# Optimization experiments

Measured on AMD Instinct MI355X. Metric: run time of the kernel, lower is better.

Reference implementation:

```python
import jax, jax.numpy as jnp
import numpy as np

N, D, C, K = 16384, 128, 10, 16
EPS = float(np.finfo(np.float32).eps)
LOG2PI = float(np.log(2.0 * np.pi))


def setup_inputs() -> dict:
    key = jax.random.key(0)
    ks = jax.random.split(key, 8)
    X = jax.random.normal(ks[0], (N, D), dtype=jnp.float32)
    y = jax.random.randint(ks[1], (N,), 0, C, dtype=jnp.int32)
    responsibilities = jax.random.uniform(ks[2], (C, N, K), dtype=jnp.float32)
    mu = jax.random.normal(ks[3], (C, K, D), dtype=jnp.float32)
    # lower < mu < upper so the truncation normalizer is positive (as after gmm_initialisation)
    lower = mu - 1.0 + 0.1 * jax.random.normal(ks[4], (C, K, D), dtype=jnp.float32)
    upper = mu + 1.0 + 0.1 * jax.random.normal(ks[5], (C, K, D), dtype=jnp.float32)
    sigma = jnp.abs(jax.random.normal(ks[6], (C, K, D), dtype=jnp.float32))
    logits_k = jax.random.normal(ks[7], (C, K), dtype=jnp.float32)
    eta = jnp.float32(0.0)  # model initializes eta = 0.0 (non-trainable)
    return {"X": X, "y": y, "responsibilities": responsibilities, "mu": mu,
            "lower": lower, "upper": upper, "sigma": sigma,
            "logits_k": logits_k, "eta": eta}


def _stgma_loss(X, y, responsibilities, mu, lower, upper, sigma, logits_k, eta):
    # scale = eps + softplus(sigma), shape [C, K, D]
    scale = EPS + jax.nn.softplus(sigma)
    # normalizing constant per (class, component): prod_d [Phi(up) - Phi(lo)] + eps
    ndtr = jax.scipy.special.ndtr
    z = ndtr((upper - mu) / scale) - ndtr((lower - mu) / scale)       # [C, K, D]
    log_norm = jnp.log(jnp.prod(z, axis=-1) + EPS)                    # [C, K]
    log_cat = jax.nn.log_softmax(logits_k, axis=-1)                   # [C, K]

    # gather per-sample class parameters: [N, K, D]
    mu_y, lo_y, up_y, sc_y = mu[y], lower[y], upper[y], scale[y]
    xk = X[:, None, :]                                                # [N, 1, D]

    # soft truncation margins: sum_d -softplus(-eta * (x - lower)) etc.
    lp_low = -jnp.sum(jax.nn.softplus(-eta * (xk - lo_y)), axis=-1)   # [N, K]
    lp_up = -jnp.sum(jax.nn.softplus(-eta * (up_y - xk)), axis=-1)    # [N, K]

    # independent diagonal Normal log prob per component
    zd = (xk - mu_y) / sc_y
    comp_lp = jnp.sum(-0.5 * zd * zd - jnp.log(sc_y), axis=-1) - 0.5 * D * LOG2PI  # [N, K]

    log_pdf = log_cat[y] - log_norm[y] + lp_low + lp_up + comp_lp     # [N, K]

    # responsibilities for each sample from its own class
    resp = responsibilities[y, jnp.arange(N)]                         # [N, K]
    weighted = resp * log_pdf                                         # [N, K]

    # per-class reduce_mean over the class's samples and components, then -sum
    onehot = (y[:, None] == jnp.arange(C)[None, :]).astype(weighted.dtype)  # [N, C]
    class_sums = jnp.einsum('nk,nc->c', weighted, onehot)             # [C]
    counts = jnp.sum(onehot, axis=0) * K                              # [C]
    return -jnp.sum(class_sums / counts)


def reference(X, y, responsibilities, mu, lower, upper, sigma, logits_k, eta):
    return _stgma_loss(X, y, responsibilities, mu, lower, upper, sigma, logits_k, eta)
```

## Files before the change

kernel.cpp:

```cpp
#include <hip/hip_runtime.h>
#include <math.h>

#define N_PTS 16384
#define D_DIM 128
#define C_CLS 10
#define K_MIX 16
#define HIST_BLOCKS 64
#define MAIN_BPC 32

constexpr float EPSF   = 1.1920928955078125e-07f;
constexpr float LOG2PI = 1.8378770664093453f;
constexpr float LN2F   = 0.6931471805599453f;

__device__ __forceinline__ float softplusf(float x) {
    if (x > 20.f)  return x;
    if (x < -20.f) return expf(x);
    return log1pf(expf(x));
}
__device__ __forceinline__ float ndtrf(float x) {
    return 0.5f * erfcf(-x * 0.70710678118654752440f);
}

__global__ __launch_bounds__(256) void k_prep(
    const float* __restrict__ mu, const float* __restrict__ lower,
    const float* __restrict__ upper, const float* __restrict__ sigma,
    const int* __restrict__ y,
    float2* __restrict__ abT, float* __restrict__ loT, float* __restrict__ upT,
    float* __restrict__ Ack, int* __restrict__ blockCnt) {
    int b = blockIdx.x, t = threadIdx.x;
    if (b < C_CLS * K_MIX) {
        int c = b / K_MIX, k = b % K_MIX;
        __shared__ float rs0[256], rs1[256], rp[256];
        float logsc = 0.f, mu2 = 0.f, zz = 1.f;
        if (t < D_DIM) {
            int gi = b * D_DIM + t;
            float m = mu[gi], lo = lower[gi], up = upper[gi], sg = sigma[gi];
            float sc = EPSF + softplusf(sg);
            float is = 1.f / sc;
            int ti = (c * D_DIM + t) * K_MIX + k;
            abT[ti] = make_float2(is * is, 2.f * m * is * is);
            loT[ti] = lo; upT[ti] = up;
            logsc = logf(sc);
            mu2   = m * m * is * is;
            zz    = ndtrf((up - m) * is) - ndtrf((lo - m) * is);
        }
        rs0[t] = logsc; rs1[t] = mu2; rp[t] = zz;
        __syncthreads();
        for (int off = 128; off > 0; off >>= 1) {
            if (t < off) { rs0[t] += rs0[t+off]; rs1[t] += rs1[t+off]; rp[t] *= rp[t+off]; }
            __syncthreads();
        }
        if (t == 0) {
            float log_norm = logf(rp[0] + EPSF);
            Ack[b] = -log_norm - rs0[0] - 0.5f * (float)D_DIM * LOG2PI - 0.5f * rs1[0];
        }
    } else {
        int h = b - C_CLS * K_MIX;
        __shared__ int hist[C_CLS];
        if (t < C_CLS) hist[t] = 0;
        __syncthreads();
        int c = y[h * 256 + t];
        int lane = t & 63;
        for (int cc = 0; cc < C_CLS; ++cc) {
            unsigned long long m = __ballot(c == cc);
            if (lane == 0 && m) atomicAdd(&hist[cc], __popcll(m));
        }
        __syncthreads();
        if (t < C_CLS) blockCnt[h * C_CLS + t] = hist[t];
    }
}

__global__ __launch_bounds__(256) void k_scatter(
    const int* __restrict__ y, const int* __restrict__ blockCnt,
    const float* __restrict__ logits, const float* __restrict__ Ack,
    int* __restrict__ idxSorted, int* __restrict__ classOff,
    float* __restrict__ invden, float* __restrict__ const_ck) {
    __shared__ int sCnt[HIST_BLOCKS * C_CLS];
    __shared__ int sClassOff[C_CLS + 1];
    __shared__ int myOff[C_CLS];
    __shared__ int wcnt[4][C_CLS];
    __shared__ int wbase[4][C_CLS];
    int h = blockIdx.x, t = threadIdx.x;
    for (int i = t; i < HIST_BLOCKS * C_CLS; i += 256) sCnt[i] = blockCnt[i];
    __syncthreads();
    if (t == 0) {
        int acc = 0;
        for (int c = 0; c < C_CLS; ++c) {
            sClassOff[c] = acc;
            int s = 0;
            for (int hh = 0; hh < HIST_BLOCKS; ++hh) s += sCnt[hh * C_CLS + c];
            acc += s;
        }
        sClassOff[C_CLS] = acc;
    }
    __syncthreads();
    if (t < C_CLS) {
        int s = sClassOff[t];
        for (int hh = 0; hh < h; ++hh) s += sCnt[hh * C_CLS + t];
        myOff[t] = s;
    }
    __syncthreads();
    int n = h * 256 + t;
    int c = y[n];
    int w = t >> 6, lane = t & 63;
    int rank = 0;
    for (int cc = 0; cc < C_CLS; ++cc) {
        unsigned long long m = __ballot(c == cc);
        if (c == cc) rank = __popcll(m & ((1ull << lane) - 1ull));
        if (lane == 0) wcnt[w][cc] = __popcll(m);
    }
    __syncthreads();
    if (t < 4 * C_CLS) {
        int ww = t / C_CLS, cc = t % C_CLS;
        int s = myOff[cc];
        for (int w2 = 0; w2 < ww; ++w2) s += wcnt[w2][cc];
        wbase[ww][cc] = s;
    }
    __syncthreads();
    idxSorted[wbase[w][c] + rank] = n;

    if (h == 0) {
        __shared__ float lse[C_CLS];
        if (t < C_CLS) {
            float mx = -1e30f;
            for (int k = 0; k < K_MIX; ++k) mx = fmaxf(mx, logits[t * K_MIX + k]);
            float se = 0.f;
            for (int k = 0; k < K_MIX; ++k) se += expf(logits[t * K_MIX + k] - mx);
            lse[t] = mx + logf(se);
            int cnt = sClassOff[t + 1] - sClassOff[t];
            invden[t] = (cnt > 0) ? 1.f / ((float)cnt * (float)K_MIX) : 0.f;
        }
        if (t < C_CLS + 1) classOff[t] = sClassOff[t];
        __syncthreads();
        if (t < C_CLS * K_MIX) const_ck[t] = logits[t] - lse[t / K_MIX] + Ack[t];
    }
}

__global__ __launch_bounds__(256) void k_main(
    const float* __restrict__ X, const float* __restrict__ resp,
    const float2* __restrict__ abT, const float* __restrict__ loT,
    const float* __restrict__ upT, const float* __restrict__ const_ck,
    const int* __restrict__ classOff, const float* __restrict__ invden,
    const int* __restrict__ idxSorted, const float* __restrict__ etap,
    float* __restrict__ partials) {
    int b = blockIdx.x;
    int c = b / MAIN_BPC, j = b % MAIN_BPC;
    int t = threadIdx.x;
    int w = t >> 6, lane = t & 63;
    int k = lane & 15, dc = lane >> 4;
    const int d0 = dc * 32;

    float a_[32], b_[32];
    const float2* ab = abT + (size_t)c * D_DIM * K_MIX + k;
    #pragma unroll
    for (int i = 0; i < 32; ++i) {
        float2 v = ab[(size_t)(d0 + i) * K_MIX];
        a_[i] = v.x; b_[i] = v.y;
    }
    float ck  = const_ck[c * K_MIX + k];
    float eta = etap[0];
    float inv = invden[c];
    int off = classOff[c];
    int cnt = classOff[c + 1] - off;
    const float lpconst = -2.f * (float)D_DIM * LN2F;

    float wsum = 0.f;
    for (int p = j * 4 + w; p < cnt; p += MAIN_BPC * 4) {
        int n = idxSorted[off + p];
        const float* xr = X + (size_t)n * D_DIM + d0;
        float acc = 0.f, lp = lpconst;
        if (eta == 0.f) {
            #pragma unroll
            for (int i4 = 0; i4 < 8; ++i4) {
                float4 xv = *reinterpret_cast<const float4*>(xr + i4 * 4);
                acc = fmaf(xv.x, fmaf(a_[i4*4+0], xv.x, -b_[i4*4+0]), acc);
                acc = fmaf(xv.y, fmaf(a_[i4*4+1], xv.y, -b_[i4*4+1]), acc);
                acc = fmaf(xv.z, fmaf(a_[i4*4+2], xv.z, -b_[i4*4+2]), acc);
                acc = fmaf(xv.w, fmaf(a_[i4*4+3], xv.w, -b_[i4*4+3]), acc);
            }
            acc += __shfl_xor(acc, 16);
            acc += __shfl_xor(acc, 32);
        } else {
            float lpp = 0.f;
            const float* lo = loT + (size_t)c * D_DIM * K_MIX + k;
            const float* up = upT + (size_t)c * D_DIM * K_MIX + k;
            #pragma unroll
            for (int i4 = 0; i4 < 8; ++i4) {
                float4 xv = *reinterpret_cast<const float4*>(xr + i4 * 4);
                float xs4[4] = {xv.x, xv.y, xv.z, xv.w};
                #pragma unroll
                for (int q = 0; q < 4; ++q) {
                    int i = i4 * 4 + q;
                    float x = xs4[q];
                    acc = fmaf(x, fmaf(a_[i], x, -b_[i]), acc);
                    float lov = lo[(size_t)(d0 + i) * K_MIX];
                    float upv = up[(size_t)(d0 + i) * K_MIX];
                    lpp -= softplusf(-eta * (x - lov)) + softplusf(-eta * (upv - x));
                }
            }
            acc += __shfl_xor(acc, 16); acc += __shfl_xor(acc, 32);
            lpp += __shfl_xor(lpp, 16); lpp += __shfl_xor(lpp, 32);
            lp = lpp;
        }
        float r = resp[((size_t)c * N_PTS + n) * K_MIX + k];
        float v = r * (ck + lp - 0.5f * acc) * inv;
        v += __shfl_xor(v, 1); v += __shfl_xor(v, 2);
        v += __shfl_xor(v, 4); v += __shfl_xor(v, 8);
        wsum += v;
    }
    __shared__ float ws[4];
    if (lane == 0) ws[w] = wsum;
    __syncthreads();
    if (t == 0) partials[b] = ws[0] + ws[1] + ws[2] + ws[3];
}

__global__ __launch_bounds__(256) void k_final(
    const float* __restrict__ partials, float* __restrict__ out) {
    __shared__ float red[256];
    int t = threadIdx.x;
    float s = 0.f;
    for (int i = t; i < C_CLS * MAIN_BPC; i += 256) s += partials[i];
    red[t] = s;
    __syncthreads();
    for (int off = 128; off > 0; off >>= 1) {
        if (t < off) red[t] += red[t + off];
        __syncthreads();
    }
    if (t == 0) out[0] = -red[0];
}

extern "C" void kernel_launch(void* const* d_in, const int* in_sizes, int n_in,
                              void* d_out, int out_size, void* d_ws, size_t ws_size,
                              hipStream_t stream) {
    const float* X      = (const float*)d_in[0];
    const int*   y      = (const int*)  d_in[1];
    const float* resp   = (const float*)d_in[2];
    const float* mu     = (const float*)d_in[3];
    const float* lower  = (const float*)d_in[4];
    const float* upper  = (const float*)d_in[5];
    const float* sigma  = (const float*)d_in[6];
    const float* logits = (const float*)d_in[7];
    const float* eta    = (const float*)d_in[8];
    float* out = (float*)d_out;

    char* ws = (char*)d_ws;
    size_t off = 0;
    auto alloc = [&](size_t bytes) {
        void* p = ws + off;
        off += (bytes + 255) & ~size_t(255);
        return p;
    };
    const size_t PE = (size_t)C_CLS * D_DIM * K_MIX;
    float2* abT      = (float2*)alloc(PE * sizeof(float2));
    float*  loT      = (float*) alloc(PE * sizeof(float));
    float*  upT      = (float*) alloc(PE * sizeof(float));
    float*  Ack      = (float*) alloc(C_CLS * K_MIX * sizeof(float));
    float*  const_ck = (float*) alloc(C_CLS * K_MIX * sizeof(float));
    int*    blockCnt = (int*)   alloc(HIST_BLOCKS * C_CLS * sizeof(int));
    int*    idxSorted= (int*)   alloc(N_PTS * sizeof(int));
    int*    classOff = (int*)   alloc((C_CLS + 1) * sizeof(int));
    float*  invden   = (float*) alloc(C_CLS * sizeof(float));
    float*  partials = (float*) alloc(C_CLS * MAIN_BPC * sizeof(float));

    k_prep<<<C_CLS * K_MIX + HIST_BLOCKS, 256, 0, stream>>>(
        mu, lower, upper, sigma, y, abT, loT, upT, Ack, blockCnt);
    k_scatter<<<HIST_BLOCKS, 256, 0, stream>>>(
        y, blockCnt, logits, Ack, idxSorted, classOff, invden, const_ck);
    k_main<<<C_CLS * MAIN_BPC, 256, 0, stream>>>(
        X, resp, abT, loT, upT, const_ck, classOff, invden, idxSorted, eta, partials);
    k_final<<<1, 256, 0, stream>>>(partials, out);
}
```

Baseline: 34.53 us.

## Fuse final reduction into main kernel and restructure per-sample accumulation

Removes the separate final-reduction kernel by having the last block of k_main (found through an atomic counter reset with a memset) sum the partials. Per-class parameters are now stored in natural [c,k,d] layout, so each lane reads its 32 coefficients contiguously. The eta==0 path processes two samples per warp iteration to gain more memory-level parallelism, and it defers the per-sample shuffle reductions to a single reduction at the end, folding the constants into a pre-scaled ck. Blocks per class drop from 32 to 28. The trade-offs are an extra memset launch and more register pressure from two sets of float4 buffers.

```diff
diff --git a/kernel.cpp b/kernel.cpp
--- a/kernel.cpp
+++ b/kernel.cpp
@@ -5,8 +5,9 @@
 #define D_DIM 128
 #define C_CLS 10
 #define K_MIX 16
-#define HIST_BLOCKS 64
-#define MAIN_BPC 32
+#define HB    64
+#define BPC   28
+#define GRID3 (C_CLS * BPC)
 
 constexpr float EPSF   = 1.1920928955078125e-07f;
 constexpr float LOG2PI = 1.8378770664093453f;
@@ -25,11 +26,10 @@
     const float* __restrict__ mu, const float* __restrict__ lower,
     const float* __restrict__ upper, const float* __restrict__ sigma,
     const int* __restrict__ y,
-    float2* __restrict__ abT, float* __restrict__ loT, float* __restrict__ upT,
+    float2* __restrict__ ab, float* __restrict__ loT, float* __restrict__ upT,
     float* __restrict__ Ack, int* __restrict__ blockCnt) {
     int b = blockIdx.x, t = threadIdx.x;
     if (b < C_CLS * K_MIX) {
-        int c = b / K_MIX, k = b % K_MIX;
         __shared__ float rs0[256], rs1[256], rp[256];
         float logsc = 0.f, mu2 = 0.f, zz = 1.f;
         if (t < D_DIM) {
@@ -37,9 +37,8 @@
             float m = mu[gi], lo = lower[gi], up = upper[gi], sg = sigma[gi];
             float sc = EPSF + softplusf(sg);
             float is = 1.f / sc;
-            int ti = (c * D_DIM + t) * K_MIX + k;
-            abT[ti] = make_float2(is * is, 2.f * m * is * is);
-            loT[ti] = lo; upT[ti] = up;
+            ab[gi]  = make_float2(is * is, 2.f * m * is * is);
+            loT[gi] = lo; upT[gi] = up;
             logsc = logf(sc);
             mu2   = m * m * is * is;
             zz    = ndtrf((up - m) * is) - ndtrf((lo - m) * is);
@@ -75,29 +74,29 @@
     const float* __restrict__ logits, const float* __restrict__ Ack,
     int* __restrict__ idxSorted, int* __restrict__ classOff,
     float* __restrict__ invden, float* __restrict__ const_ck) {
-    __shared__ int sCnt[HIST_BLOCKS * C_CLS];
-    __shared__ int sClassOff[C_CLS + 1];
-    __shared__ int myOff[C_CLS];
+    __shared__ int sCnt[HB * C_CLS];
+    __shared__ int sOff[C_CLS + 1];
+    __shared__ int sMyOff[C_CLS];
     __shared__ int wcnt[4][C_CLS];
     __shared__ int wbase[4][C_CLS];
     int h = blockIdx.x, t = threadIdx.x;
-    for (int i = t; i < HIST_BLOCKS * C_CLS; i += 256) sCnt[i] = blockCnt[i];
+    for (int i = t; i < HB * C_CLS; i += 256) sCnt[i] = blockCnt[i];
     __syncthreads();
     if (t == 0) {
         int acc = 0;
         for (int c = 0; c < C_CLS; ++c) {
-            sClassOff[c] = acc;
+            sOff[c] = acc;
             int s = 0;
-            for (int hh = 0; hh < HIST_BLOCKS; ++hh) s += sCnt[hh * C_CLS + c];
+            for (int hh = 0; hh < HB; ++hh) s += sCnt[hh * C_CLS + c];
             acc += s;
         }
-        sClassOff[C_CLS] = acc;
+        sOff[C_CLS] = acc;
     }
     __syncthreads();
     if (t < C_CLS) {
-        int s = sClassOff[t];
+        int s = sOff[t];
         for (int hh = 0; hh < h; ++hh) s += sCnt[hh * C_CLS + t];
-        myOff[t] = s;
+        sMyOff[t] = s;
     }
     __syncthreads();
     int n = h * 256 + t;
@@ -112,7 +111,7 @@
     __syncthreads();
     if (t < 4 * C_CLS) {
         int ww = t / C_CLS, cc = t % C_CLS;
-        int s = myOff[cc];
+        int s = sMyOff[cc];
         for (int w2 = 0; w2 < ww; ++w2) s += wcnt[w2][cc];
         wbase[ww][cc] = s;
     }
@@ -127,10 +126,10 @@
             float se = 0.f;
             for (int k = 0; k < K_MIX; ++k) se += expf(logits[t * K_MIX + k] - mx);
             lse[t] = mx + logf(se);
-            int cnt = sClassOff[t + 1] - sClassOff[t];
+            int cnt = sOff[t + 1] - sOff[t];
             invden[t] = (cnt > 0) ? 1.f / ((float)cnt * (float)K_MIX) : 0.f;
         }
-        if (t < C_CLS + 1) classOff[t] = sClassOff[t];
+        if (t < C_CLS + 1) classOff[t] = sOff[t];
         __syncthreads();
         if (t < C_CLS * K_MIX) const_ck[t] = logits[t] - lse[t / K_MIX] + Ack[t];
     }
@@ -138,95 +137,133 @@
 
 __global__ __launch_bounds__(256) void k_main(
     const float* __restrict__ X, const float* __restrict__ resp,
-    const float2* __restrict__ abT, const float* __restrict__ loT,
+    const float2* __restrict__ ab, const float* __restrict__ loT,
     const float* __restrict__ upT, const float* __restrict__ const_ck,
     const int* __restrict__ classOff, const float* __restrict__ invden,
     const int* __restrict__ idxSorted, const float* __restrict__ etap,
-    float* __restrict__ partials) {
-    int b = blockIdx.x;
-    int c = b / MAIN_BPC, j = b % MAIN_BPC;
-    int t = threadIdx.x;
-    int w = t >> 6, lane = t & 63;
-    int k = lane & 15, dc = lane >> 4;
+    float* __restrict__ partials, int* __restrict__ done,
+    float* __restrict__ out) {
+    const int b = blockIdx.x, t = threadIdx.x;
+    const int w = t >> 6, lane = t & 63;
+    const int k = lane & 15, dc = lane >> 4;
     const int d0 = dc * 32;
+    const int c = b / BPC, j = b % BPC;
+
+    __shared__ float sW[4];
+    __shared__ int   sLast;
 
     float a_[32], b_[32];
-    const float2* ab = abT + (size_t)c * D_DIM * K_MIX + k;
-    #pragma unroll
-    for (int i = 0; i < 32; ++i) {
-        float2 v = ab[(size_t)(d0 + i) * K_MIX];
-        a_[i] = v.x; b_[i] = v.y;
-    }
-    float ck  = const_ck[c * K_MIX + k];
-    float eta = etap[0];
-    float inv = invden[c];
-    int off = classOff[c];
-    int cnt = classOff[c + 1] - off;
+    {
+        const float2* p = ab + ((size_t)(c * K_MIX + k)) * D_DIM + d0;
+        #pragma unroll
+        for (int i = 0; i < 32; ++i) { float2 v = p[i]; a_[i] = v.x; b_[i] = v.y; }
+    }
+    const float eta = etap[0];
     const float lpconst = -2.f * (float)D_DIM * LN2F;
+    const float ck4 = 0.25f * (const_ck[c * K_MIX + k] + (eta == 0.f ? lpconst : 0.f));
+    const float inv = invden[c];
+    const int off = classOff[c];
+    const int cnt = classOff[c + 1] - off;
 
     float wsum = 0.f;
-    for (int p = j * 4 + w; p < cnt; p += MAIN_BPC * 4) {
-        int n = idxSorted[off + p];
-        const float* xr = X + (size_t)n * D_DIM + d0;
-        float acc = 0.f, lp = lpconst;
-        if (eta == 0.f) {
-            #pragma unroll
-            for (int i4 = 0; i4 < 8; ++i4) {
-                float4 xv = *reinterpret_cast<const float4*>(xr + i4 * 4);
-                acc = fmaf(xv.x, fmaf(a_[i4*4+0], xv.x, -b_[i4*4+0]), acc);
-                acc = fmaf(xv.y, fmaf(a_[i4*4+1], xv.y, -b_[i4*4+1]), acc);
-                acc = fmaf(xv.z, fmaf(a_[i4*4+2], xv.z, -b_[i4*4+2]), acc);
-                acc = fmaf(xv.w, fmaf(a_[i4*4+3], xv.w, -b_[i4*4+3]), acc);
-            }
-            acc += __shfl_xor(acc, 16);
-            acc += __shfl_xor(acc, 32);
-        } else {
-            float lpp = 0.f;
-            const float* lo = loT + (size_t)c * D_DIM * K_MIX + k;
-            const float* up = upT + (size_t)c * D_DIM * K_MIX + k;
-            #pragma unroll
-            for (int i4 = 0; i4 < 8; ++i4) {
-                float4 xv = *reinterpret_cast<const float4*>(xr + i4 * 4);
-                float xs4[4] = {xv.x, xv.y, xv.z, xv.w};
+    if (eta == 0.f) {
+        for (int base = j * 64; base < cnt; base += BPC * 64) {
+            int rem = cnt - base; if (rem > 64) rem = 64;
+            for (int i = w; i < rem; i += 8) {
+                int i1 = i + 4;
+                bool has1 = (i1 < rem);
+                int n0 = idxSorted[off + base + i];
+                int n1 = idxSorted[off + base + (has1 ? i1 : i)];
+                const float4* x0 = reinterpret_cast<const float4*>(X + (size_t)n0 * D_DIM + d0);
+                const float4* x1 = reinterpret_cast<const float4*>(X + (size_t)n1 * D_DIM + d0);
+                float4 va[8], vb[8];
                 #pragma unroll
-                for (int q = 0; q < 4; ++q) {
-                    int i = i4 * 4 + q;
-                    float x = xs4[q];
-                    acc = fmaf(x, fmaf(a_[i], x, -b_[i]), acc);
-                    float lov = lo[(size_t)(d0 + i) * K_MIX];
-                    float upv = up[(size_t)(d0 + i) * K_MIX];
-                    lpp -= softplusf(-eta * (x - lov)) + softplusf(-eta * (upv - x));
+                for (int q = 0; q < 8; ++q) va[q] = x0[q];
+                #pragma unroll
+                for (int q = 0; q < 8; ++q) vb[q] = x1[q];
+                float r0 = resp[((size_t)c * N_PTS + n0) * K_MIX + k];
+                float r1 = resp[((size_t)c * N_PTS + n1) * K_MIX + k];
+                float acc0 = 0.f, acc1 = 0.f;
+                #pragma unroll
+                for (int q = 0; q < 8; ++q) {
+                    acc0 = fmaf(va[q].x, fmaf(a_[q*4+0], va[q].x, -b_[q*4+0]), acc0);
+                    acc0 = fmaf(va[q].y, fmaf(a_[q*4+1], va[q].y, -b_[q*4+1]), acc0);
+                    acc0 = fmaf(va[q].z, fmaf(a_[q*4+2], va[q].z, -b_[q*4+2]), acc0);
+                    acc0 = fmaf(va[q].w, fmaf(a_[q*4+3], va[q].w, -b_[q*4+3]), acc0);
+                    acc1 = fmaf(vb[q].x, fmaf(a_[q*4+0], vb[q].x, -b_[q*4+0]), acc1);
+                    acc1 = fmaf(vb[q].y, fmaf(a_[q*4+1], vb[q].y, -b_[q*4+1]), acc1);
+                    acc1 = fmaf(vb[q].z, fmaf(a_[q*4+2], vb[q].z, -b_[q*4+2]), acc1);
+                    acc1 = fmaf(vb[q].w, fmaf(a_[q*4+3], vb[q].w, -b_[q*4+3]), acc1);
+                }
+                float v0 = fmaf(-0.5f, acc0, ck4);
+                wsum = fmaf(r0, v0, wsum);
+                if (has1) {
+                    float v1 = fmaf(-0.5f, acc1, ck4);
+                    wsum = fmaf(r1, v1, wsum);
                 }
             }
-            acc += __shfl_xor(acc, 16); acc += __shfl_xor(acc, 32);
-            lpp += __shfl_xor(lpp, 16); lpp += __shfl_xor(lpp, 32);
-            lp = lpp;
-        }
-        float r = resp[((size_t)c * N_PTS + n) * K_MIX + k];
-        float v = r * (ck + lp - 0.5f * acc) * inv;
-        v += __shfl_xor(v, 1); v += __shfl_xor(v, 2);
-        v += __shfl_xor(v, 4); v += __shfl_xor(v, 8);
-        wsum += v;
-    }
-    __shared__ float ws[4];
-    if (lane == 0) ws[w] = wsum;
-    __syncthreads();
-    if (t == 0) partials[b] = ws[0] + ws[1] + ws[2] + ws[3];
-}
-
-__global__ __launch_bounds__(256) void k_final(
-    const float* __restrict__ partials, float* __restrict__ out) {
-    __shared__ float red[256];
-    int t = threadIdx.x;
-    float s = 0.f;
-    for (int i = t; i < C_CLS * MAIN_BPC; i += 256) s += partials[i];
-    red[t] = s;
-    __syncthreads();
-    for (int off = 128; off > 0; off >>= 1) {
-        if (t < off) red[t] += red[t + off];
-        __syncthreads();
-    }
-    if (t == 0) out[0] = -red[0];
+        }
+    } else {
+        const float4* lo4 = reinterpret_cast<const float4*>(loT + ((size_t)(c * K_MIX + k)) * D_DIM + d0);
+        const float4* up4 = reinterpret_cast<const float4*>(upT + ((size_t)(c * K_MIX + k)) * D_DIM + d0);
+        const float lpc4 = 0.25f * lpconst * 0.f;
+        (void)lpc4;
+        for (int base = j * 64; base < cnt; base += BPC * 64) {
+            int rem = cnt - base; if (rem > 64) rem = 64;
+            for (int i = w; i < rem; i += 4) {
+                int n = idxSorted[off + base + i];
+                const float4* xr = reinterpret_cast<const float4*>(X + (size_t)n * D_DIM + d0);
+                float r = resp[((size_t)c * N_PTS + n) * K_MIX + k];
+                float acc = 0.f, lpp = 0.f;
+                #pragma unroll
+                for (int q = 0; q < 8; ++q) {
+                    float4 xv = xr[q];
+                    float4 lv = lo4[q];
+                    float4 uv = up4[q];
+                    float x4[4] = {xv.x, xv.y, xv.z, xv.w};
+                    float l4[4] = {lv.x, lv.y, lv.z, lv.w};
+                    float u4[4] = {uv.x, uv.y, uv.z, uv.w};
+                    #pragma unroll
+                    for (int qq = 0; qq < 4; ++qq) {
+                        float x = x4[qq];
+                        acc = fmaf(x, fmaf(a_[q*4+qq], x, -b_[q*4+qq]), acc);
+                        lpp -= softplusf(-eta * (x - l4[qq]))
+                             + softplusf(-eta * (u4[qq] - x));
+                    }
+                }
+                float v = fmaf(-0.5f, acc, ck4 + lpp);
+                wsum = fmaf(r, v, wsum);
+            }
+        }
+    }
+    wsum *= inv;
+
+    #pragma unroll
+    for (int o = 1; o < 64; o <<= 1) wsum += __shfl_xor(wsum, o);
+    if (lane == 0) sW[w] = wsum;
+    __syncthreads();
+    if (t == 0) {
+        partials[b] = sW[0] + sW[1] + sW[2] + sW[3];
+        __threadfence();
+        int prev = __hip_atomic_fetch_add(done, 1, __ATOMIC_ACQ_REL,
+                                          __HIP_MEMORY_SCOPE_AGENT);
+        sLast = (prev == GRID3 - 1);
+    }
+    __syncthreads();
+
+    if (sLast) {
+        __threadfence();
+        __shared__ float red[256];
+        float s = partials[t];
+        if (t < GRID3 - 256) s += partials[256 + t];
+        red[t] = s;
+        __syncthreads();
+        for (int o = 128; o > 0; o >>= 1) {
+            if (t < o) red[t] += red[t + o];
+            __syncthreads();
+        }
+        if (t == 0) out[0] = -red[0];
+    }
 }
 
 extern "C" void kernel_launch(void* const* d_in, const int* in_sizes, int n_in,
@@ -244,29 +281,31 @@
     float* out = (float*)d_out;
 
     char* ws = (char*)d_ws;
-    size_t off = 0;
+    size_t off = 256;
     auto alloc = [&](size_t bytes) {
         void* p = ws + off;
         off += (bytes + 255) & ~size_t(255);
         return p;
     };
-    const size_t PE = (size_t)C_CLS * D_DIM * K_MIX;
-    float2* abT      = (float2*)alloc(PE * sizeof(float2));
+    const size_t PE = (size_t)C_CLS * K_MIX * D_DIM;
+    int*    done     = (int*)ws;
+    float2* ab       = (float2*)alloc(PE * sizeof(float2));
     float*  loT      = (float*) alloc(PE * sizeof(float));
     float*  upT      = (float*) alloc(PE * sizeof(float));
     float*  Ack      = (float*) alloc(C_CLS * K_MIX * sizeof(float));
     float*  const_ck = (float*) alloc(C_CLS * K_MIX * sizeof(float));
-    int*    blockCnt = (int*)   alloc(HIST_BLOCKS * C_CLS * sizeof(int));
+    int*    blockCnt = (int*)   alloc(HB * C_CLS * sizeof(int));
     int*    idxSorted= (int*)   alloc(N_PTS * sizeof(int));
     int*    classOff = (int*)   alloc((C_CLS + 1) * sizeof(int));
     float*  invden   = (float*) alloc(C_CLS * sizeof(float));
-    float*  partials = (float*) alloc(C_CLS * MAIN_BPC * sizeof(float));
-
-    k_prep<<<C_CLS * K_MIX + HIST_BLOCKS, 256, 0, stream>>>(
-        mu, lower, upper, sigma, y, abT, loT, upT, Ack, blockCnt);
-    k_scatter<<<HIST_BLOCKS, 256, 0, stream>>>(
+    float*  partials = (float*) alloc(GRID3 * sizeof(float));
+
+    hipMemsetAsync(done, 0, sizeof(int), stream);
+    k_prep<<<C_CLS * K_MIX + HB, 256, 0, stream>>>(
+        mu, lower, upper, sigma, y, ab, loT, upT, Ack, blockCnt);
+    k_scatter<<<HB, 256, 0, stream>>>(
         y, blockCnt, logits, Ack, idxSorted, classOff, invden, const_ck);
-    k_main<<<C_CLS * MAIN_BPC, 256, 0, stream>>>(
-        X, resp, abT, loT, upT, const_ck, classOff, invden, idxSorted, eta, partials);
-    k_final<<<1, 256, 0, stream>>>(partials, out);
-}
+    k_main<<<GRID3, 256, 0, stream>>>(
+        X, resp, ab, loT, upT, const_ck, classOff, invden, idxSorted, eta,
+        partials, done, out);
+}
```

After: 47.20 us. +36.7%, slower.
